# Kernel tuning notes

Measured on AMD Instinct MI355X. Metric: run time of the kernel, lower is better.

The kernel has to match this reference:

```python
import jax, jax.numpy as jnp
import numpy as np

B, T, E, H = 4, 1024, 2048, 32
D = E // H

def setup_inputs() -> dict:
    key = jax.random.key(0)
    ks = jax.random.split(key, 10)
    s = 0.02
    hidden_states = jax.random.normal(ks[0], (B, T, E), dtype=jnp.float32)
    # additive causal mask, HF-OPT style: 0 on/below diagonal, finfo.min above
    neg = jnp.finfo(jnp.float32).min
    tril = jnp.tril(jnp.ones((T, T), dtype=bool))
    attention_mask = jnp.where(tril, 0.0, neg)[None, None, :, :] * jnp.ones((B, 1, 1, 1), jnp.float32)
    Wq = jax.random.normal(ks[1], (E, E), jnp.float32) * s
    bq = jnp.zeros((E,), jnp.float32)
    Wk = jax.random.normal(ks[2], (E, E), jnp.float32) * s
    bk = jnp.zeros((E,), jnp.float32)
    Wv = jax.random.normal(ks[3], (E, E), jnp.float32) * s
    bv = jnp.zeros((E,), jnp.float32)
    Wo = jax.random.normal(ks[4], (E, E), jnp.float32) * s
    bo = jnp.zeros((E,), jnp.float32)
    return {"hidden_states": hidden_states, "attention_mask": attention_mask,
            "Wq": Wq, "bq": bq, "Wk": Wk, "bk": bk, "Wv": Wv, "bv": bv, "Wo": Wo, "bo": bo}

def reference(hidden_states, attention_mask, Wq, bq, Wk, bk, Wv, bv, Wo, bo):
    scaling = D ** -0.5
    # torch nn.Linear: y = x @ W.T + b
    q = (hidden_states @ Wq.T + bq) * scaling          # [B,T,E]
    k = hidden_states @ Wk.T + bk
    v = hidden_states @ Wv.T + bv
    def shape(x):
        return x.reshape(B, T, H, D).transpose(0, 2, 1, 3)  # [B,H,T,D]
    q, k, v = shape(q), shape(k), shape(v)
    attn = jnp.einsum('bhqd,bhkd->bhqk', q, k)          # [B,H,T,T]
    attn = attn + attention_mask                        # broadcast over heads
    attn = jnp.maximum(attn, jnp.finfo(attn.dtype).min) # min-clamp as in source
    attn = jax.nn.softmax(attn, axis=-1)
    out = jnp.einsum('bhqk,bhkd->bhqd', attn, v)        # [B,H,T,D]
    out = out.transpose(0, 2, 1, 3).reshape(B, T, E)
    return out @ Wo.T + bo
```

## Files before the change

kernel.cpp:

```cpp
#include <hip/hip_runtime.h>

typedef __attribute__((ext_vector_type(8))) short short8;
typedef __attribute__((ext_vector_type(4))) float floatx4;
typedef unsigned short u16;
typedef unsigned int u32;

constexpr int kB = 4, kT = 1024, kE = 2048, kH = 32, kD = 64;
constexpr int kBT = kB * kT;
constexpr size_t kHeadSz = (size_t)kB * kH * kT * kD;
constexpr size_t kWSz = (size_t)kE * kE;

__device__ __forceinline__ u16 f2bf(float f) {
  union { float f; u32 u; } x; x.f = f;
  u32 r = x.u + 0x7FFFu + ((x.u >> 16) & 1u);
  return (u16)(r >> 16);
}

#define GLDS16(g, l) __builtin_amdgcn_global_load_lds( \
    (const __attribute__((address_space(1))) void*)(g), \
    (__attribute__((address_space(3))) void*)(l), 16, 0, 0)

__global__ __launch_bounds__(256) void cvt_bf16(const float* __restrict__ s0, u16* __restrict__ d0,
                                                const float* __restrict__ s1, u16* __restrict__ d1,
                                                const float* __restrict__ s2, u16* __restrict__ d2,
                                                const float* __restrict__ s3, u16* __restrict__ d3,
                                                const float* __restrict__ s4, u16* __restrict__ d4) {
  const float* src; u16* dst; size_t n;
  switch (blockIdx.y) {
    case 0: src = s0; dst = d0; n = (size_t)kBT * kE; break;
    case 1: src = s1; dst = d1; n = kWSz; break;
    case 2: src = s2; dst = d2; n = kWSz; break;
    case 3: src = s3; dst = d3; n = kWSz; break;
    default: src = s4; dst = d4; n = kWSz; break;
  }
  const size_t stride = (size_t)gridDim.x * blockDim.x * 8;
  for (size_t i = ((size_t)blockIdx.x * blockDim.x + threadIdx.x) * 8; i < n; i += stride) {
    float4 a = *(const float4*)(src + i);
    float4 b = *(const float4*)(src + i + 4);
    union { u16 h[8]; uint4 v; } u;
    u.h[0] = f2bf(a.x); u.h[1] = f2bf(a.y); u.h[2] = f2bf(a.z); u.h[3] = f2bf(a.w);
    u.h[4] = f2bf(b.x); u.h[5] = f2bf(b.y); u.h[6] = f2bf(b.z); u.h[7] = f2bf(b.w);
    *(uint4*)(dst + i) = u.v;
  }
}

__device__ __forceinline__ void gemm128(const u16* __restrict__ Ag,
                                        const u16* __restrict__ Bg,
                                        u16* As, u16* Bs, floatx4 acc[4][4]) {
  const int tid = threadIdx.x;
  const int wave = tid >> 6, lane = tid & 63;
  const int quad = lane >> 4, m16 = lane & 15;
  const int wm = wave >> 1, wn = wave & 1;
  const int lr = lane >> 3;
  const int swc = ((lane & 7) ^ lr) * 8;
  const int x7 = m16 & 7;
#pragma unroll
  for (int i = 0; i < 4; ++i)
#pragma unroll
    for (int j = 0; j < 4; ++j) acc[i][j] = (floatx4){0.f, 0.f, 0.f, 0.f};

  for (int kt = 0; kt < kE / 64; ++kt) {
    const int k0 = kt * 64;
#pragma unroll
    for (int i = 0; i < 4; ++i) {
      const int r = wave * 32 + i * 8;
      GLDS16(Ag + (size_t)(r + lr) * kE + k0 + swc, As + r * 64);
      GLDS16(Bg + (size_t)(r + lr) * kE + k0 + swc, Bs + r * 64);
    }
    __syncthreads();
#pragma unroll
    for (int kk = 0; kk < 2; ++kk) {
      short8 af[4], bf[4];
#pragma unroll
      for (int i = 0; i < 4; ++i)
        af[i] = *(const short8*)(As + (wm * 64 + i * 16 + m16) * 64 + (((kk * 4 + quad) ^ x7) * 8));
#pragma unroll
      for (int i = 0; i < 4; ++i)
        bf[i] = *(const short8*)(Bs + (wn * 64 + i * 16 + m16) * 64 + (((kk * 4 + quad) ^ x7) * 8));
#pragma unroll
      for (int im = 0; im < 4; ++im)
#pragma unroll
        for (int in = 0; in < 4; ++in)
          acc[im][in] = __builtin_amdgcn_mfma_f32_16x16x32_bf16(af[im], bf[in], acc[im][in], 0, 0, 0);
    }
    __syncthreads();
  }
}

__global__ __launch_bounds__(256) void qkv_gemm(
    const u16* __restrict__ hs,
    const u16* __restrict__ Wq, const float* __restrict__ bq,
    const u16* __restrict__ Wk, const float* __restrict__ bk,
    const u16* __restrict__ Wv, const float* __restrict__ bv,
    u16* __restrict__ qkv) {
  __shared__ __align__(16) u16 As[128 * 64];
  __shared__ __align__(16) u16 Bs[128 * 64];
  const int z = blockIdx.z;
  const u16* W      = (z == 0) ? Wq : (z == 1) ? Wk : Wv;
  const float* bias = (z == 0) ? bq : (z == 1) ? bk : bv;
  const float scale = (z == 0) ? 0.125f : 1.0f;
  const int m0 = blockIdx.y * 128, n0 = blockIdx.x * 128;
  floatx4 acc[4][4];
  gemm128(hs + (size_t)m0 * kE, W + (size_t)n0 * kE, As, Bs, acc);

  const int tid = threadIdx.x, wave = tid >> 6, lane = tid & 63;
  const int quad = lane >> 4, m16 = lane & 15, wm = wave >> 1, wn = wave & 1;
#pragma unroll
  for (int in = 0; in < 4; ++in) {
    const int ng = n0 + wn * 64 + in * 16 + m16;
    const float bn = bias[ng];
    const int h = ng >> 6, d = ng & 63;
#pragma unroll
    for (int im = 0; im < 4; ++im) {
      const int mg0 = m0 + wm * 64 + im * 16 + quad * 4;
#pragma unroll
      for (int r = 0; r < 4; ++r) {
        const int m = mg0 + r;
        const int bb = m >> 10, t = m & 1023;
        qkv[((((size_t)z * kB + bb) * kH + h) << 16) + (size_t)t * 64 + d] =
            f2bf((acc[im][in][r] + bn) * scale);
      }
    }
  }
}

__global__ __launch_bounds__(256) void attn_fwd(
    const u16* __restrict__ qg, const u16* __restrict__ kg,
    const u16* __restrict__ vg, u16* __restrict__ og) {
  __shared__ __align__(16) u16 Ks[64 * 72];
  __shared__ __align__(16) u16 Vt[64 * 64];
  __shared__ __align__(16) u16 Ps[4][16 * 72];
  const int bb = blockIdx.z, h = blockIdx.y;
  const int qt = gridDim.x - 1 - blockIdx.x;
  const int q0 = qt * 128;
  const int tid = threadIdx.x, wave = tid >> 6, lane = tid & 63;
  const int quad = lane >> 4, m16 = lane & 15;
  const size_t base = ((size_t)(bb * kH + h)) << 16;

  short8 qf[2][2];
#pragma unroll
  for (int st = 0; st < 2; ++st)
#pragma unroll
    for (int kk = 0; kk < 2; ++kk)
      qf[st][kk] = *(const short8*)(qg + base +
          (size_t)(q0 + st * 64 + wave * 16 + m16) * 64 + kk * 32 + quad * 8);

  floatx4 oacc[2][4];
  float li[2][4];
#pragma unroll
  for (int st = 0; st < 2; ++st)
#pragma unroll
    for (int j = 0; j < 4; ++j) {
      oacc[st][j] = (floatx4){0.f, 0.f, 0.f, 0.f};
      li[st][j] = 0.f;
    }

  const int kr = tid >> 3, kc = (tid & 7) * 8;
  const int rp = kr * 2;
  const int nk = 2 * qt + 2;

  uint4 ka0 = *(const uint4*)(kg + base + (size_t)kr * 64 + kc);
  uint4 ka1 = *(const uint4*)(kg + base + (size_t)(kr + 32) * 64 + kc);
  uint4 va0 = *(const uint4*)(vg + base + (size_t)rp * 64 + kc);
  uint4 va1 = *(const uint4*)(vg + base + (size_t)(rp + 1) * 64 + kc);

  for (int kt = 0; kt < nk; ++kt) {
    __syncthreads();
    *(uint4*)(Ks + kr * 72 + kc) = ka0;
    *(uint4*)(Ks + (kr + 32) * 72 + kc) = ka1;
    {
      const u16* pa = (const u16*)&va0;
      const u16* pb = (const u16*)&va1;
      u32* vtw = (u32*)Vt;
      const int gw = rp >> 3, wq = (rp & 7) >> 1;
#pragma unroll
      for (int j = 0; j < 8; ++j) {
        const int d = kc + j;
        vtw[d * 32 + ((gw ^ ((d >> 3) & 7)) << 2) + wq] = (u32)pa[j] | ((u32)pb[j] << 16);
      }
    }
    __syncthreads();
    if (kt + 1 < nk) {
      const u16* kb = kg + base + (size_t)(kt + 1) * 64 * 64;
      ka0 = *(const uint4*)(kb + (size_t)kr * 64 + kc);
      ka1 = *(const uint4*)(kb + (size_t)(kr + 32) * 64 + kc);
      const u16* vb = vg + base + (size_t)(kt + 1) * 64 * 64;
      va0 = *(const uint4*)(vb + (size_t)rp * 64 + kc);
      va1 = *(const uint4*)(vb + (size_t)(rp + 1) * 64 + kc);
    }
#pragma unroll
    for (int st = 0; st < 2; ++st) {
      if (kt > 2 * qt + st) continue;
      floatx4 s[4];
#pragma unroll
      for (int jn = 0; jn < 4; ++jn) {
        s[jn] = (floatx4){0.f, 0.f, 0.f, 0.f};
#pragma unroll
        for (int kk = 0; kk < 2; ++kk) {
          short8 kf = *(const short8*)(Ks + (jn * 16 + m16) * 72 + kk * 32 + quad * 8);
          s[jn] = __builtin_amdgcn_mfma_f32_16x16x32_bf16(qf[st][kk], kf, s[jn], 0, 0, 0);
        }
      }
      if (kt == 2 * qt + st) {
        const int row0 = q0 + st * 64 + wave * 16 + quad * 4;
#pragma unroll
        for (int jn = 0; jn < 4; ++jn) {
          const int key = kt * 64 + jn * 16 + m16;
#pragma unroll
          for (int r = 0; r < 4; ++r)
            if (key > row0 + r) s[jn][r] = -1e30f;
        }
      }
      u16* ps = Ps[wave];
#pragma unroll
      for (int jn = 0; jn < 4; ++jn)
#pragma unroll
        for (int r = 0; r < 4; ++r) {
          const float p = __expf(s[jn][r] - 9.0f);
          li[st][r] += p;
          ps[(quad * 4 + r) * 72 + jn * 16 + m16] = f2bf(p);
        }
      asm volatile("s_waitcnt lgkmcnt(0)" ::: "memory");
      short8 pf[2];
#pragma unroll
      for (int kk = 0; kk < 2; ++kk)
        pf[kk] = *(const short8*)(ps + m16 * 72 + kk * 32 + quad * 8);
#pragma unroll
      for (int jd = 0; jd < 4; ++jd) {
        const int dswz = (jd * 2 + (m16 >> 3)) & 7;
#pragma unroll
        for (int kk = 0; kk < 2; ++kk) {
          short8 vf = *(const short8*)(Vt + (jd * 16 + m16) * 64 + ((kk * 4 + quad) ^ dswz) * 8);
          oacc[st][jd] = __builtin_amdgcn_mfma_f32_16x16x32_bf16(pf[kk], vf, oacc[st][jd], 0, 0, 0);
        }
      }
    }
  }
#pragma unroll
  for (int st = 0; st < 2; ++st)
#pragma unroll
    for (int r = 0; r < 4; ++r)
#pragma unroll
      for (int off = 8; off >= 1; off >>= 1)
        li[st][r] += __shfl_xor(li[st][r], off);
#pragma unroll
  for (int st = 0; st < 2; ++st)
#pragma unroll
    for (int jd = 0; jd < 4; ++jd) {
      const int d = jd * 16 + m16;
#pragma unroll
      for (int r = 0; r < 4; ++r) {
        const int t = q0 + st * 64 + wave * 16 + quad * 4 + r;
        og[((size_t)bb * kT + t) * kE + h * 64 + d] =
            f2bf(oacc[st][jd][r] / fmaxf(li[st][r], 1e-30f));
      }
    }
}

__global__ __launch_bounds__(256) void out_gemm(
    const u16* __restrict__ ao, const u16* __restrict__ Wo,
    const float* __restrict__ bo, float* __restrict__ out) {
  __shared__ __align__(16) u16 As[128 * 64];
  __shared__ __align__(16) u16 Bs[128 * 64];
  const int m0 = blockIdx.y * 128, n0 = blockIdx.x * 128;
  floatx4 acc[4][4];
  gemm128(ao + (size_t)m0 * kE, Wo + (size_t)n0 * kE, As, Bs, acc);

  const int tid = threadIdx.x, wave = tid >> 6, lane = tid & 63;
  const int quad = lane >> 4, m16 = lane & 15, wm = wave >> 1, wn = wave & 1;
#pragma unroll
  for (int in = 0; in < 4; ++in) {
    const int ng = n0 + wn * 64 + in * 16 + m16;
    const float bn = bo[ng];
#pragma unroll
    for (int im = 0; im < 4; ++im) {
      const int mg0 = m0 + wm * 64 + im * 16 + quad * 4;
#pragma unroll
      for (int r = 0; r < 4; ++r)
        out[(size_t)(mg0 + r) * kE + ng] = acc[im][in][r] + bn;
    }
  }
}

extern "C" void kernel_launch(void* const* d_in, const int* in_sizes, int n_in,
                              void* d_out, int out_size, void* d_ws, size_t ws_size,
                              hipStream_t stream) {
  (void)in_sizes; (void)n_in; (void)out_size; (void)ws_size;
  const float* hs = (const float*)d_in[0];
  const float* Wq = (const float*)d_in[2];
  const float* bq = (const float*)d_in[3];
  const float* Wk = (const float*)d_in[4];
  const float* bk = (const float*)d_in[5];
  const float* Wv = (const float*)d_in[6];
  const float* bv = (const float*)d_in[7];
  const float* Wo = (const float*)d_in[8];
  const float* bo = (const float*)d_in[9];
  u16* ws = (u16*)d_ws;
  u16* hsb = ws;
  u16* Wqb = hsb + (size_t)kBT * kE;
  u16* Wkb = Wqb + kWSz;
  u16* Wvb = Wkb + kWSz;
  u16* Wob = Wvb + kWSz;
  u16* q   = Wob + kWSz;
  u16* k   = q + kHeadSz;
  u16* v   = k + kHeadSz;
  u16* ao  = v + kHeadSz;

  cvt_bf16<<<dim3(1024, 5), 256, 0, stream>>>(hs, hsb, Wq, Wqb, Wk, Wkb, Wv, Wvb, Wo, Wob);
  qkv_gemm<<<dim3(kE / 128, kBT / 128, 3), 256, 0, stream>>>(hsb, Wqb, bq, Wkb, bk, Wvb, bv, q);
  attn_fwd<<<dim3(kT / 128, kH, kB), 256, 0, stream>>>(q, k, v, ao);
  out_gemm<<<dim3(kE / 128, kBT / 128), 256, 0, stream>>>(ao, Wob, bo, (float*)d_out);
}
```

Before: 404.7 us.

## Triple-buffer GEMM with 128x256 tiles, split MFMA phases and async prefetch

Result: faster. 392.7 us (-3.0%).

```diff
diff --git a/kernel.cpp b/kernel.cpp
--- a/kernel.cpp
+++ b/kernel.cpp
@@ -10,6 +10,10 @@
 constexpr size_t kHeadSz = (size_t)kB * kH * kT * kD;
 constexpr size_t kWSz = (size_t)kE * kE;
 
+constexpr int BM = 128, BN = 256, BK = 64;
+constexpr int NT = kE / BK;
+static_assert(NT == 32, "pipeline peel assumes NT==32");
+
 __device__ __forceinline__ u16 f2bf(float f) {
   union { float f; u32 u; } x; x.f = f;
   u32 r = x.u + 0x7FFFu + ((x.u >> 16) & 1u);
@@ -19,6 +23,12 @@
 #define GLDS16(g, l) __builtin_amdgcn_global_load_lds( \
     (const __attribute__((address_space(1))) void*)(g), \
     (__attribute__((address_space(3))) void*)(l), 16, 0, 0)
+
+__device__ __forceinline__ void bar() {
+  asm volatile("" ::: "memory");
+  __builtin_amdgcn_s_barrier();
+  asm volatile("" ::: "memory");
+}
 
 __global__ __launch_bounds__(256) void cvt_bf16(const float* __restrict__ s0, u16* __restrict__ d0,
                                                 const float* __restrict__ s1, u16* __restrict__ d1,
@@ -44,67 +54,145 @@
   }
 }
 
-__device__ __forceinline__ void gemm128(const u16* __restrict__ Ag,
-                                        const u16* __restrict__ Bg,
-                                        u16* As, u16* Bs, floatx4 acc[4][4]) {
+
+__device__ __forceinline__ void stage_tile(const u16* __restrict__ Ag,
+                                           const u16* __restrict__ Bg,
+                                           u16* Asd, u16* Bsd, int k0,
+                                           int wave, int lr, int swc) {
+#pragma unroll
+  for (int i = 0; i < 2; ++i) {
+    const int r = wave * 16 + i * 8;
+    GLDS16(Ag + (size_t)(r + lr) * kE + k0 + swc, Asd + r * 64);
+  }
+#pragma unroll
+  for (int i = 0; i < 4; ++i) {
+    const int r = wave * 32 + i * 8;
+    GLDS16(Bg + (size_t)(r + lr) * kE + k0 + swc, Bsd + r * 64);
+  }
+}
+
+template <int VM, bool STAGE>
+__device__ __forceinline__ void ktile(const u16* __restrict__ Ag,
+                                      const u16* __restrict__ Bg, int k0n,
+                                      u16* Asc, u16* Bsc, u16* Asn, u16* Bsn,
+                                      floatx4 acc[4][4]) {
   const int tid = threadIdx.x;
   const int wave = tid >> 6, lane = tid & 63;
-  const int quad = lane >> 4, m16 = lane & 15;
-  const int wm = wave >> 1, wn = wave & 1;
-  const int lr = lane >> 3;
-  const int swc = ((lane & 7) ^ lr) * 8;
-  const int x7 = m16 & 7;
+  const int quad = lane >> 4, m16 = lane & 15, x7 = m16 & 7;
+  const int wm = wave >> 2, wn = wave & 3;
+  const int lr = lane >> 3, swc = ((lane & 7) ^ lr) * 8;
+
+  asm volatile("s_waitcnt vmcnt(%0)" :: "i"(VM) : "memory");
+  bar();
+  __builtin_amdgcn_sched_barrier(0);
+
+  short8 af[4][2], bf[2][2];
+#pragma unroll
+  for (int im = 0; im < 4; ++im)
+#pragma unroll
+    for (int kk = 0; kk < 2; ++kk)
+      af[im][kk] = *(const short8*)(Asc + (wm * 64 + im * 16 + m16) * 64 +
+                                    (((kk * 4 + quad) ^ x7) * 8));
+#pragma unroll
+  for (int in = 0; in < 2; ++in)
+#pragma unroll
+    for (int kk = 0; kk < 2; ++kk)
+      bf[in][kk] = *(const short8*)(Bsc + (wn * 64 + in * 16 + m16) * 64 +
+                                    (((kk * 4 + quad) ^ x7) * 8));
+  if constexpr (STAGE) {
+#pragma unroll
+    for (int i = 0; i < 2; ++i) {
+      const int r = wave * 16 + i * 8;
+      GLDS16(Ag + (size_t)(r + lr) * kE + k0n + swc, Asn + r * 64);
+    }
+    GLDS16(Bg + (size_t)(wave * 32 + lr) * kE + k0n + swc, Bsn + wave * 32 * 64);
+  }
+  bar();
+  __builtin_amdgcn_s_setprio(1);
+#pragma unroll
+  for (int im = 0; im < 4; ++im)
+#pragma unroll
+    for (int in = 0; in < 2; ++in)
+#pragma unroll
+      for (int kk = 0; kk < 2; ++kk)
+        acc[im][in] = __builtin_amdgcn_mfma_f32_16x16x32_bf16(af[im][kk], bf[in][kk],
+                                                              acc[im][in], 0, 0, 0);
+  __builtin_amdgcn_s_setprio(0);
+  bar();
+
+  short8 bf2[2][2];
+#pragma unroll
+  for (int in = 0; in < 2; ++in)
+#pragma unroll
+    for (int kk = 0; kk < 2; ++kk)
+      bf2[in][kk] = *(const short8*)(Bsc + (wn * 64 + (in + 2) * 16 + m16) * 64 +
+                                     (((kk * 4 + quad) ^ x7) * 8));
+  if constexpr (STAGE) {
+#pragma unroll
+    for (int i = 1; i < 4; ++i) {
+      const int r = wave * 32 + i * 8;
+      GLDS16(Bg + (size_t)(r + lr) * kE + k0n + swc, Bsn + r * 64);
+    }
+  }
+  bar();
+  __builtin_amdgcn_s_setprio(1);
+#pragma unroll
+  for (int im = 0; im < 4; ++im)
+#pragma unroll
+    for (int in = 0; in < 2; ++in)
+#pragma unroll
+      for (int kk = 0; kk < 2; ++kk)
+        acc[im][in + 2] = __builtin_amdgcn_mfma_f32_16x16x32_bf16(af[im][kk], bf2[in][kk],
+                                                                  acc[im][in + 2], 0, 0, 0);
+  __builtin_amdgcn_s_setprio(0);
+  asm volatile("s_waitcnt lgkmcnt(0)" ::: "memory");
+  bar();
+}
+
+__device__ __forceinline__ void gemm_pipe(const u16* __restrict__ Ag,
+                                          const u16* __restrict__ Bg,
+                                          u16 (*As)[BM * 64], u16 (*Bs)[BN * 64],
+                                          floatx4 acc[4][4]) {
+  const int tid = threadIdx.x;
+  const int wave = tid >> 6, lane = tid & 63;
+  const int lr = lane >> 3, swc = ((lane & 7) ^ lr) * 8;
 #pragma unroll
   for (int i = 0; i < 4; ++i)
 #pragma unroll
     for (int j = 0; j < 4; ++j) acc[i][j] = (floatx4){0.f, 0.f, 0.f, 0.f};
 
-  for (int kt = 0; kt < kE / 64; ++kt) {
-    const int k0 = kt * 64;
-#pragma unroll
-    for (int i = 0; i < 4; ++i) {
-      const int r = wave * 32 + i * 8;
-      GLDS16(Ag + (size_t)(r + lr) * kE + k0 + swc, As + r * 64);
-      GLDS16(Bg + (size_t)(r + lr) * kE + k0 + swc, Bs + r * 64);
-    }
-    __syncthreads();
-#pragma unroll
-    for (int kk = 0; kk < 2; ++kk) {
-      short8 af[4], bf[4];
-#pragma unroll
-      for (int i = 0; i < 4; ++i)
-        af[i] = *(const short8*)(As + (wm * 64 + i * 16 + m16) * 64 + (((kk * 4 + quad) ^ x7) * 8));
-#pragma unroll
-      for (int i = 0; i < 4; ++i)
-        bf[i] = *(const short8*)(Bs + (wn * 64 + i * 16 + m16) * 64 + (((kk * 4 + quad) ^ x7) * 8));
-#pragma unroll
-      for (int im = 0; im < 4; ++im)
-#pragma unroll
-        for (int in = 0; in < 4; ++in)
-          acc[im][in] = __builtin_amdgcn_mfma_f32_16x16x32_bf16(af[im], bf[in], acc[im][in], 0, 0, 0);
-    }
-    __syncthreads();
-  }
-}
-
-__global__ __launch_bounds__(256) void qkv_gemm(
+  stage_tile(Ag, Bg, As[0], Bs[0], 0 * BK, wave, lr, swc);
+  stage_tile(Ag, Bg, As[1], Bs[1], 1 * BK, wave, lr, swc);
+
+#pragma unroll 1
+  for (int i = 0; i < NT - 2; i += 3) {
+    ktile<6, true>(Ag, Bg, (i + 2) * BK, As[0], Bs[0], As[2], Bs[2], acc);
+    ktile<6, true>(Ag, Bg, (i + 3) * BK, As[1], Bs[1], As[0], Bs[0], acc);
+    ktile<6, true>(Ag, Bg, (i + 4) * BK, As[2], Bs[2], As[1], Bs[1], acc);
+  }
+  ktile<6, false>(Ag, Bg, 0, As[0], Bs[0], nullptr, nullptr, acc);
+  ktile<0, false>(Ag, Bg, 0, As[1], Bs[1], nullptr, nullptr, acc);
+}
+
+__global__ __launch_bounds__(512, 2) void qkv_gemm(
     const u16* __restrict__ hs,
     const u16* __restrict__ Wq, const float* __restrict__ bq,
     const u16* __restrict__ Wk, const float* __restrict__ bk,
     const u16* __restrict__ Wv, const float* __restrict__ bv,
     u16* __restrict__ qkv) {
-  __shared__ __align__(16) u16 As[128 * 64];
-  __shared__ __align__(16) u16 Bs[128 * 64];
+  __shared__ __align__(16) u16 As[3][BM * 64];
+  __shared__ __align__(16) u16 Bs[3][BN * 64];
   const int z = blockIdx.z;
   const u16* W      = (z == 0) ? Wq : (z == 1) ? Wk : Wv;
   const float* bias = (z == 0) ? bq : (z == 1) ? bk : bv;
   const float scale = (z == 0) ? 0.125f : 1.0f;
-  const int m0 = blockIdx.y * 128, n0 = blockIdx.x * 128;
+  const int m0 = blockIdx.y * BM, n0 = blockIdx.x * BN;
   floatx4 acc[4][4];
-  gemm128(hs + (size_t)m0 * kE, W + (size_t)n0 * kE, As, Bs, acc);
+  gemm_pipe(hs + (size_t)m0 * kE, W + (size_t)n0 * kE, As, Bs, acc);
 
   const int tid = threadIdx.x, wave = tid >> 6, lane = tid & 63;
-  const int quad = lane >> 4, m16 = lane & 15, wm = wave >> 1, wn = wave & 1;
+  const int quad = lane >> 4, m16 = lane & 15;
+  const int wm = wave >> 2, wn = wave & 3;
 #pragma unroll
   for (int in = 0; in < 4; ++in) {
     const int ng = n0 + wn * 64 + in * 16 + m16;
@@ -257,17 +345,18 @@
     }
 }
 
-__global__ __launch_bounds__(256) void out_gemm(
+__global__ __launch_bounds__(512, 2) void out_gemm(
     const u16* __restrict__ ao, const u16* __restrict__ Wo,
     const float* __restrict__ bo, float* __restrict__ out) {
-  __shared__ __align__(16) u16 As[128 * 64];
-  __shared__ __align__(16) u16 Bs[128 * 64];
-  const int m0 = blockIdx.y * 128, n0 = blockIdx.x * 128;
+  __shared__ __align__(16) u16 As[3][BM * 64];
+  __shared__ __align__(16) u16 Bs[3][BN * 64];
+  const int m0 = blockIdx.y * BM, n0 = blockIdx.x * BN;
   floatx4 acc[4][4];
-  gemm128(ao + (size_t)m0 * kE, Wo + (size_t)n0 * kE, As, Bs, acc);
+  gemm_pipe(ao + (size_t)m0 * kE, Wo + (size_t)n0 * kE, As, Bs, acc);
 
   const int tid = threadIdx.x, wave = tid >> 6, lane = tid & 63;
-  const int quad = lane >> 4, m16 = lane & 15, wm = wave >> 1, wn = wave & 1;
+  const int quad = lane >> 4, m16 = lane & 15;
+  const int wm = wave >> 2, wn = wave & 3;
 #pragma unroll
   for (int in = 0; in < 4; ++in) {
     const int ng = n0 + wn * 64 + in * 16 + m16;
@@ -307,7 +396,7 @@
   u16* ao  = v + kHeadSz;
 
   cvt_bf16<<<dim3(1024, 5), 256, 0, stream>>>(hs, hsb, Wq, Wqb, Wk, Wkb, Wv, Wvb, Wo, Wob);
-  qkv_gemm<<<dim3(kE / 128, kBT / 128, 3), 256, 0, stream>>>(hsb, Wqb, bq, Wkb, bk, Wvb, bv, q);
+  qkv_gemm<<<dim3(kE / BN, kBT / BM, 3), 512, 0, stream>>>(hsb, Wqb, bq, Wkb, bk, Wvb, bv, q);
   attn_fwd<<<dim3(kT / 128, kH, kB), 256, 0, stream>>>(q, k, v, ao);
-  out_gemm<<<dim3(kE / 128, kBT / 128), 256, 0, stream>>>(ao, Wob, bo, (float*)d_out);
-}
+  out_gemm<<<dim3(kE / BN, kBT / BM), 512, 0, stream>>>(ao, Wob, bo, (float*)d_out);
+}
```
